# Optimization experiments

Measured on AMD Instinct MI355X. Metric: run time of the kernel, lower is better.

## Reference

```python
import jax, jax.numpy as jnp
import numpy as np

B_, N_, D_ = 8, 1024, 64
H_, DH_ = 4, 16
DI_, DS_, DTR_ = 128, 64, 4
MAXP = 512


def _ln(x, w, b, eps=1e-5):
    m = jnp.mean(x, -1, keepdims=True)
    v = jnp.mean((x - m) ** 2, -1, keepdims=True)
    return (x - m) * jax.lax.rsqrt(v + eps) * w + b


def _attn(x, drop_mask, Wq, Wkv, Wo, bo, rel_emb):
    b, n, d = x.shape
    scale = DH_ ** -0.5
    q = (x @ Wq).reshape(b, n, H_, DH_).transpose(0, 2, 1, 3)
    kv = x @ Wkv
    k = kv[..., :d].reshape(b, n, H_, DH_).transpose(0, 2, 1, 3)
    v = kv[..., d:].reshape(b, n, H_, DH_).transpose(0, 2, 1, 3)
    dots = jnp.einsum('bhid,bhjd->bhij', q, k) * scale
    seq = jnp.arange(n)
    dist = jnp.clip(seq[:, None] - seq[None, :], -MAXP, MAXP) + MAXP
    rpe = rel_emb[dist]  # (n, n, DH_)
    dots = dots + jnp.einsum('bhid,ijd->bhij', q, rpe) * scale
    # stochastic key drop: Bernoulli(0.3) positions get -1e12
    dots = dots + drop_mask.astype(dots.dtype) * (-1e12)
    attn = jax.nn.softmax(dots, axis=-1)
    out = jnp.einsum('bhij,bhjd->bhid', attn, v)
    out = out.transpose(0, 2, 1, 3).reshape(b, n, H_ * DH_)
    return out @ Wo + bo


def _mamba(x, W_in, conv_w, conv_b, W_xproj, W_dt, b_dt, A_log, Dm, W_out):
    b, n, _ = x.shape
    xz = x @ W_in                      # (b, n, 2*DI_)
    u, z = xz[..., :DI_], xz[..., DI_:]
    uc = u.transpose(0, 2, 1)          # (b, DI_, n)
    uc = jax.lax.conv_general_dilated(
        uc, conv_w[:, None, :], (1,), ((3, 0),),
        feature_group_count=DI_, dimension_numbers=('NCH', 'OIH', 'NCH'))
    uc = uc + conv_b[None, :, None]
    u = jax.nn.silu(uc).transpose(0, 2, 1)  # (b, n, DI_)
    xdb = u @ W_xproj                  # (b, n, DTR_+2*DS_)
    dt = jax.nn.softplus(xdb[..., :DTR_] @ W_dt + b_dt)  # (b, n, DI_)
    Bm = xdb[..., DTR_:DTR_ + DS_]
    Cm = xdb[..., DTR_ + DS_:]
    A = -jnp.exp(A_log)                # (DI_, DS_)

    def step(h, inp):
        dt_t, B_t, C_t, u_t = inp      # (b,DI_),(b,DS_),(b,DS_),(b,DI_)
        dA = jnp.exp(dt_t[..., None] * A)
        h = h * dA + (dt_t * u_t)[..., None] * B_t[:, None, :]
        y = jnp.einsum('bds,bs->bd', h, C_t)
        return h, y

    h0 = jnp.zeros((b, DI_, DS_), x.dtype)
    xs = (dt.transpose(1, 0, 2), Bm.transpose(1, 0, 2),
          Cm.transpose(1, 0, 2), u.transpose(1, 0, 2))
    _, ys = jax.lax.scan(step, h0, xs)
    y = ys.transpose(1, 0, 2) + u * Dm
    y = y * jax.nn.silu(z)
    return y @ W_out


def _rmsgn(x, gamma, eps=1e-5, groups=4):
    shp = x.shape
    dpg = shp[-1] // groups
    xg = x.reshape(shp[:-1] + (groups, dpg))
    rms = jnp.sqrt(jnp.sum(xg * xg, -1, keepdims=True)) * (dpg ** -0.5)
    return (xg / (rms + eps)).reshape(shp) * gamma


def _ff1(x, c1_w, c1_b, d1_w, d1_b):
    # SwiGLUConvDeconv1d(64, 256, kernel=4, shift=1); x: (b, s2, 64)
    s2 = x.shape[1]
    xc = x.transpose(0, 2, 1)
    xc = jnp.pad(xc, ((0, 0), (0, 0), (3, 3)))
    xc = jax.lax.conv_general_dilated(
        xc, c1_w, (1,), 'VALID', dimension_numbers=('NCH', 'OIH', 'NCH'))
    xc = xc + c1_b[None, :, None]
    gate = jax.nn.silu(xc[:, 256:, :])
    xc = xc[:, :256, :] * gate
    # ConvTranspose1d stride 1 == conv with flipped kernel, full padding
    w = jnp.flip(d1_w, -1).transpose(1, 0, 2)  # (64, 256, 4)
    xc = jax.lax.conv_general_dilated(
        xc, w, (1,), ((3, 3),), dimension_numbers=('NCH', 'OIH', 'NCH'))
    xc = xc + d1_b[None, :, None]
    out = xc.transpose(0, 2, 1)
    return out[:, 3:3 + s2, :]


def _forward(x, drop_mask, ln1_w, ln1_b, Wq, Wkv, Wo, bo, rel_emb,
             ln2_w, ln2_b, W_in, conv_w, conv_b, W_xproj, W_dt, b_dt,
             A_log, Dm, W_out, gamma, c1_w, c1_b, d1_w, d1_b, ln3_w, ln3_b):
    xt = _ln(x, ln1_w, ln1_b)
    xt = _attn(xt, drop_mask, Wq, Wkv, Wo, bo, rel_emb) + x
    x = x + xt  # dropout p=0 -> identity (faithful to original residual math)
    xt = _ln(x, ln2_w, ln2_b)
    m = _mamba(xt, W_in, conv_w, conv_b, W_xproj, W_dt, b_dt, A_log, Dm, W_out)
    m = jnp.where(m >= 0, m, 0.01 * m)  # leaky_relu
    m = _rmsgn(m, gamma)
    m = m + 0.5 * _ff1(m, c1_w, c1_b, d1_w, d1_b)
    x = x + m
    return _ln(x, ln3_w, ln3_b)


def setup_inputs() -> dict:
    ks = jax.random.split(jax.random.key(0), 16)
    g = lambda i, shp, s: jax.random.normal(ks[i], shp, dtype=jnp.float32) * s
    A_log = jnp.log(jnp.tile(jnp.arange(1, DS_ + 1, dtype=jnp.float32)[None, :], (DI_, 1)))
    return {
        'x': jax.random.normal(ks[0], (B_, N_, D_), dtype=jnp.float32),
        'drop_mask': jax.random.bernoulli(ks[1], 0.3, (B_, H_, N_, N_)),
        'ln1_w': jnp.ones((D_,), jnp.float32), 'ln1_b': jnp.zeros((D_,), jnp.float32),
        'Wq': g(2, (D_, D_), 0.1), 'Wkv': g(3, (D_, 2 * D_), 0.1),
        'Wo': g(4, (D_, D_), 0.1), 'bo': jnp.zeros((D_,), jnp.float32),
        'rel_emb': g(5, (2 * MAXP + 1, DH_), 0.02),
        'ln2_w': jnp.ones((D_,), jnp.float32), 'ln2_b': jnp.zeros((D_,), jnp.float32),
        'W_in': g(6, (D_, 2 * DI_), 0.1),
        'conv_w': g(7, (DI_, 4), 0.2), 'conv_b': jnp.zeros((DI_,), jnp.float32),
        'W_xproj': g(8, (DI_, DTR_ + 2 * DS_), 0.1),
        'W_dt': g(9, (DTR_, DI_), 0.1), 'b_dt': jnp.zeros((DI_,), jnp.float32),
        'A_log': A_log, 'Dm': jnp.ones((DI_,), jnp.float32),
        'W_out': g(10, (DI_, D_), 0.1),
        'gamma': jnp.ones((D_,), jnp.float32),
        'c1_w': g(11, (512, 64, 4), 0.1), 'c1_b': jnp.zeros((512,), jnp.float32),
        'd1_w': g(12, (256, 64, 4), 0.1), 'd1_b': jnp.zeros((64,), jnp.float32),
        'ln3_w': jnp.ones((D_,), jnp.float32), 'ln3_b': jnp.zeros((D_,), jnp.float32),
    }


def reference(x, drop_mask, ln1_w, ln1_b, Wq, Wkv, Wo, bo, rel_emb,
              ln2_w, ln2_b, W_in, conv_w, conv_b, W_xproj, W_dt, b_dt,
              A_log, Dm, W_out, gamma, c1_w, c1_b, d1_w, d1_b, ln3_w, ln3_b):
    return _forward(x, drop_mask, ln1_w, ln1_b, Wq, Wkv, Wo, bo, rel_emb,
                    ln2_w, ln2_b, W_in, conv_w, conv_b, W_xproj, W_dt, b_dt,
                    A_log, Dm, W_out, gamma, c1_w, c1_b, d1_w, d1_b, ln3_w, ln3_b)
```

## Files before the change

kernel.cpp:

```cpp
#include <hip/hip_runtime.h>
#include <math.h>


__device__ __forceinline__ float wsum64(float v){
#pragma unroll
  for(int m=32;m>0;m>>=1) v += __shfl_xor(v, m, 64);
  return v;
}
__device__ __forceinline__ float wmax64(float v){
#pragma unroll
  for(int m=32;m>0;m>>=1) v = fmaxf(v, __shfl_xor(v, m, 64));
  return v;
}
__device__ __forceinline__ float silu_f(float x){ return x / (1.f + __expf(-x)); }

__global__ __launch_bounds__(256) void k_ln1_qkv(
    const float* __restrict__ x, const float* __restrict__ w1, const float* __restrict__ b1,
    const float* __restrict__ Wq, const float* __restrict__ Wkv,
    const float* __restrict__ rel, const float* __restrict__ c1w,
    const int* __restrict__ dmask,
    float* __restrict__ qb, float2* __restrict__ kvT,
    float* __restrict__ relT, float* __restrict__ c1wT,
    unsigned long long* __restrict__ mask64){
  int tid = threadIdx.x;
  if (blockIdx.x >= 2048){
    size_t base = (size_t)(blockIdx.x - 2048) * 16384;
    const int* dp = dmask + base;
    unsigned long long* mp = mask64 + (base >> 6);
#pragma unroll 4
    for(int r=0;r<64;++r){
      int m = dp[r*256 + tid];
      unsigned long long bal = __ballot(m != 0);
      if ((tid & 63) == 0) mp[r*4 + (tid >> 6)] = bal;
    }
    return;
  }
  int lane = tid & 63, warp = tid >> 6;
  int token = blockIdx.x*4 + warp;
  __shared__ float xt[4][64];
  float xv = x[(size_t)token*64 + lane];
  float mean = wsum64(xv) * 0.015625f;
  float dlt = xv - mean;
  float var = wsum64(dlt*dlt) * 0.015625f;
  float xn = dlt * rsqrtf(var + 1e-5f) * w1[lane] + b1[lane];
  xt[warp][lane] = xn;
  __syncthreads();
  float aq=0.f, ak=0.f, av=0.f;
#pragma unroll 4
  for(int dd=0; dd<64; ++dd){
    float xd = xt[warp][dd];
    aq += xd * Wq[dd*64 + lane];
    ak += xd * Wkv[dd*128 + lane];
    av += xd * Wkv[dd*128 + 64 + lane];
  }
  int b = token >> 10, i = token & 1023;
  int h = lane >> 4, dh = lane & 15;
  size_t o  = (((size_t)(b*4 + h))*1024 + i)*16 + dh;
  size_t oT = (((size_t)(b*4 + h))*16 + dh)*1024 + i;
  qb[o]=aq;
  kvT[oT] = make_float2(ak, av);

  if (blockIdx.x < 65){
    int idx = blockIdx.x*256 + tid;
    if (idx < 16*1025){
      int c = idx / 1025;
      int d = idx - c*1025;
      relT[idx] = rel[d*16 + c];
    }
  } else if (blockIdx.x < 577){
    int idx = (blockIdx.x-65)*256 + tid;
    int row = idx >> 9;
    int ii  = idx & 511;
    c1wT[idx] = c1w[(size_t)ii*256 + row];
  }
}

__global__ __launch_bounds__(256) void k_kmax(
    const float2* __restrict__ kvT, float* __restrict__ Kmax){
  int tid = threadIdx.x;
  int bh = blockIdx.x;
  const float2* base = kvT + (size_t)bh*16*1024;
  float mx = 0.f;
#pragma unroll
  for(int r=0;r<4;++r){
    int j = tid + 256*r;
    float ss = 0.f;
#pragma unroll
    for(int c=0;c<16;++c){ float2 kv = base[c*1024 + j]; ss += kv.x*kv.x; }
    mx = fmaxf(mx, ss);
  }
  mx = wmax64(mx);
  __shared__ float red[4];
  int lane = tid&63, wv = tid>>6;
  if(lane==0) red[wv]=mx;
  __syncthreads();
  if(tid==0) Kmax[bh] = sqrtf(fmaxf(fmaxf(red[0],red[1]),fmaxf(red[2],red[3])));
}

__global__ __launch_bounds__(128, 2) void k_attn(
    const float* __restrict__ qb, const float2* __restrict__ kvT,
    const unsigned long long* __restrict__ mask64, const float* __restrict__ relT,
    const float* __restrict__ Kmax, float* __restrict__ attn_raw){
  int tid = threadIdx.x;
  int lane = tid & 63, wv = tid >> 6;
  int wg   = blockIdx.x;
  int xcd  = wg & 7;
  int slot = wg >> 3;
  int bh   = xcd*4 + (slot >> 7);
  int i0   = (slot & 127) * 8;
  int b = bh >> 2, h = bh & 3;
  int R0 = wv*4, R1 = R0+1, R2 = R0+2, R3 = R0+3;

  __shared__ float Gc[8][1032];
  __shared__ float qs[8][16];
  __shared__ float G0s[8], G1024s[8];
  __shared__ float gmS[8];
  __shared__ float Ms[8];
  __shared__ float sums[8];

  {
    int r = tid >> 4, c = tid & 15;
    qs[r][c] = qb[((size_t)bh*1024 + i0 + r)*16 + c] * 0.25f;
  }
  __syncthreads();

#pragma unroll 1
  for(int bb=0; bb<9; ++bb){
    int d = tid + 128*bb;
    if (d <= 1024){
      float rl[16];
#pragma unroll
      for(int c=0;c<16;++c) rl[c] = relT[c*1025 + d];
#pragma unroll
      for(int r=0;r<8;++r){
        float g = 0.f;
#pragma unroll
        for(int c=0;c<16;++c) g += qs[r][c]*rl[c];
        if (d == 0)        G0s[r] = g;
        else if (d == 1024) G1024s[r] = g;
        else {
          int j = i0 + r + 512 - d;
          if (j >= 0 && j < 1024) Gc[r][j] = g;
        }
      }
    }
  }
  __syncthreads();
  {
    const unsigned long long* mrow = mask64 + ((size_t)bh*1024 + i0)*16;
#pragma unroll 1
    for(int r=0;r<8;++r){
      float g0 = G0s[r], g1 = G1024s[r];
      int lo = i0 + r - 512;
      int hi = i0 + r + 512;
#pragma unroll
      for(int p=0;p<8;++p){
        int j = tid + 128*p;
        unsigned long long w = mrow[r*16 + (j>>6)];
        float g;
        if (j >= hi) g = g0;
        else if (j <= lo) g = g1;
        else g = Gc[r][j];
        if ((w >> (j & 63)) & 1ULL) g = -1e30f;
        Gc[r][j] = g;
      }
    }
  }
  __syncthreads();
  {
    int r = tid >> 4, l4 = tid & 15;
    float gm = -3.0e38f;
#pragma unroll
    for(int k=0;k<64;++k) gm = fmaxf(gm, Gc[r][l4 + 16*k]);
#pragma unroll
    for(int m=1;m<16;m<<=1) gm = fmaxf(gm, __shfl_xor(gm, m, 64));
    if (l4 == 0) gmS[r] = gm;
  }
  __syncthreads();
  if (tid < 8){
    float qn = 0.f;
#pragma unroll
    for(int c=0;c<16;++c) qn += qs[tid][c]*qs[tid][c];
    Ms[tid] = gmS[tid] + sqrtf(qn)*Kmax[bh];
  }
  __syncthreads();

  float q0[16], q1[16], q2[16], q3[16];
#pragma unroll
  for(int c=0;c<16;++c){ q0[c]=qs[R0][c]; q1[c]=qs[R1][c]; q2[c]=qs[R2][c]; q3[c]=qs[R3][c]; }
  float M0 = Ms[R0], M1 = Ms[R1], M2 = Ms[R2], M3 = Ms[R3];

  const float2* kvb = kvT + (size_t)bh*16*1024;

  float s0=0.f, s1=0.f, s2=0.f, s3=0.f;
  float a0[16], a1[16], a2[16], a3[16];
#pragma unroll
  for(int c=0;c<16;++c){ a0[c]=0.f; a1[c]=0.f; a2[c]=0.f; a3[c]=0.f; }

  float2 kvA[16], kvB[16];
  int j = lane;
#pragma unroll
  for(int c=0;c<16;++c) kvA[c] = kvb[c*1024 + j];

#define ATTN_STEP(KV, JJ) do {                                              \
    float sv0 = Gc[R0][JJ], sv1 = Gc[R1][JJ], sv2 = Gc[R2][JJ], sv3 = Gc[R3][JJ]; \
    _Pragma("unroll")                                                       \
    for(int c=0;c<16;++c){                                                  \
      float kx = KV[c].x;                                                   \
      sv0 += q0[c]*kx; sv1 += q1[c]*kx; sv2 += q2[c]*kx; sv3 += q3[c]*kx;   \
    }                                                                       \
    float p0 = __expf(sv0 - M0), p1 = __expf(sv1 - M1);                     \
    float p2 = __expf(sv2 - M2), p3 = __expf(sv3 - M3);                     \
    s0 += p0; s1 += p1; s2 += p2; s3 += p3;                                 \
    _Pragma("unroll")                                                       \
    for(int c=0;c<16;++c){                                                  \
      float vy = KV[c].y;                                                   \
      a0[c] += p0*vy; a1[c] += p1*vy; a2[c] += p2*vy; a3[c] += p3*vy;       \
    }                                                                       \
  } while(0)

#pragma unroll 1
  for(int t=0;t<16;t+=2){
    int jb = (j + 64) & 1023;
#pragma unroll
    for(int c=0;c<16;++c) kvB[c] = kvb[c*1024 + jb];
    ATTN_STEP(kvA, j);
    int ja = (jb + 64) & 1023;
#pragma unroll
    for(int c=0;c<16;++c) kvA[c] = kvb[c*1024 + ja];
    ATTN_STEP(kvB, jb);
    j = ja;
  }
#undef ATTN_STEP

  s0 = wsum64(s0); s1 = wsum64(s1); s2 = wsum64(s2); s3 = wsum64(s3);
#pragma unroll
  for(int c=0;c<16;++c){
    float x0 = a0[c]; x0 += __shfl_xor(x0,32,64); x0 += __shfl_xor(x0,16,64); a0[c] = x0;
    float x1 = a1[c]; x1 += __shfl_xor(x1,32,64); x1 += __shfl_xor(x1,16,64); a1[c] = x1;
    float x2 = a2[c]; x2 += __shfl_xor(x2,32,64); x2 += __shfl_xor(x2,16,64); a2[c] = x2;
    float x3 = a3[c]; x3 += __shfl_xor(x3,32,64); x3 += __shfl_xor(x3,16,64); a3[c] = x3;
  }
  __syncthreads();
  float* red = &Gc[0][0];
  if (lane < 16){
#pragma unroll
    for(int c=0;c<16;++c){
      red[R0*272 + lane*17 + c] = a0[c];
      red[R1*272 + lane*17 + c] = a1[c];
      red[R2*272 + lane*17 + c] = a2[c];
      red[R3*272 + lane*17 + c] = a3[c];
    }
  }
  if (lane == 0){ sums[R0]=s0; sums[R1]=s1; sums[R2]=s2; sums[R3]=s3; }
  __syncthreads();
  {
    int row = tid >> 4, c = tid & 15;
    float tot = 0.f;
#pragma unroll
    for(int g=0; g<16; ++g) tot += red[row*272 + g*17 + c];
    attn_raw[((size_t)b*1024 + i0 + row)*64 + h*16 + c] = tot / sums[row];
  }
}

__global__ __launch_bounds__(256) void k_post_attn(
    const float* __restrict__ x, const float* __restrict__ attn_raw,
    const float* __restrict__ Wo, const float* __restrict__ bo,
    const float* __restrict__ ln2w, const float* __restrict__ ln2b,
    const float* __restrict__ W_in,
    float* __restrict__ x2, float* __restrict__ u0, float* __restrict__ zsarr){
  int tid = threadIdx.x;
  int lane = tid & 63, wv = tid >> 6;
  int tok0 = blockIdx.x * 16;
  __shared__ float arS[16][64];
  __shared__ float lnS[16][64];
  for(int l = tid; l < 1024; l += 256)
    arS[l >> 6][l & 63] = attn_raw[(size_t)tok0*64 + l];
  __syncthreads();
#pragma unroll 1
  for(int tt = 0; tt < 4; ++tt){
    int tl = wv*4 + tt;
    int token = tok0 + tl;
    float acc = bo[lane];
#pragma unroll 4
    for(int dd = 0; dd < 64; ++dd) acc += arS[tl][dd] * Wo[dd*64 + lane];
    float t = 2.f*x[(size_t)token*64 + lane] + acc;
    x2[(size_t)token*64 + lane] = t;
    float mean = wsum64(t)*0.015625f;
    float dlt = t - mean;
    float var = wsum64(dlt*dlt)*0.015625f;
    lnS[tl][lane] = dlt*rsqrtf(var+1e-5f)*ln2w[lane] + ln2b[lane];
  }
  __syncthreads();
  int oc = tid;
  float w[64];
#pragma unroll
  for(int dd = 0; dd < 64; ++dd) w[dd] = W_in[dd*256 + oc];
  const float4* lnS4 = (const float4*)&lnS[0][0];
#pragma unroll 1
  for(int tl = 0; tl < 16; ++tl){
    float acc = 0.f;
#pragma unroll
    for(int d4 = 0; d4 < 16; ++d4){
      float4 l4 = lnS4[tl*16 + d4];
      acc += l4.x*w[4*d4] + l4.y*w[4*d4+1] + l4.z*w[4*d4+2] + l4.w*w[4*d4+3];
    }
    int token = tok0 + tl;
    if (oc < 128) u0[(size_t)token*128 + oc] = acc;
    else          zsarr[(size_t)token*128 + (oc-128)] = silu_f(acc);
  }
}

__global__ __launch_bounds__(256) void k_conv_proj(
    const float* __restrict__ u0, const float* __restrict__ conv_w, const float* __restrict__ conv_b,
    const float* __restrict__ W_xproj, const float* __restrict__ W_dt, const float* __restrict__ b_dt,
    float* __restrict__ uarr, float* __restrict__ Bmp, float* __restrict__ Cmp, float* __restrict__ dtarr){
  int sub = threadIdx.x >> 7, c = threadIdx.x & 127;
  int token = blockIdx.x*2 + sub;
  int b = token >> 10, i = token & 1023;
  __shared__ float us[2][128];
  __shared__ float dtin[2][4];
  float acc = conv_b[c];
#pragma unroll
  for(int k2=0;k2<4;++k2){
    int t2 = i - 3 + k2;
    if (t2 >= 0) acc += u0[((size_t)b*1024 + t2)*128 + c]*conv_w[c*4+k2];
  }
  float uv = silu_f(acc);
  uarr[(size_t)token*128 + c] = uv;
  us[sub][c] = uv;
  __syncthreads();
  float accA = 0.f, accB = 0.f;
  int cB = 128 + (c & 3);
#pragma unroll 4
  for(int dd=0; dd<128; ++dd){
    float xd = us[sub][dd];
    accA += xd * W_xproj[dd*132 + c];
    accB += xd * W_xproj[dd*132 + cB];
  }
  if (c < 4){ dtin[sub][c] = accA; Cmp[(size_t)token*64 + 60 + c] = accB; }
  else if (c < 68) Bmp[(size_t)token*64 + (c-4)] = accA;
  else             Cmp[(size_t)token*64 + (c-68)] = accA;
  __syncthreads();
  float dv = b_dt[c];
#pragma unroll
  for(int r2=0;r2<4;++r2) dv += dtin[sub][r2]*W_dt[r2*128 + c];
  dv = fmaxf(dv, 0.f) + log1pf(expf(-fabsf(dv)));
  dtarr[(size_t)token*128 + c] = dv;
}

__global__ __launch_bounds__(256) void k_scan_a(
    const float* __restrict__ dtarr, const float* __restrict__ uarr,
    const float* __restrict__ Bmp, const float* __restrict__ A_log,
    float* __restrict__ Parr, float* __restrict__ Rarr){
  int lane = threadIdx.x & 63, warp = threadIdx.x >> 6;
  int w = blockIdx.x*4 + warp;
  int c = w & 7, d = (w >> 3) & 127, b = w >> 10;
  float A = -expf(A_log[d*64 + lane]);
  int tb = c*128;
  const float* dtp = dtarr + ((size_t)b*1024 + tb)*128 + d;
  const float* up  = uarr  + ((size_t)b*1024 + tb)*128 + d;
  const float* Bp  = Bmp   + ((size_t)b*1024 + tb)*64 + lane;
  float R = 0.f, sdt = 0.f;
  for(int t0=0; t0<128; t0+=8){
    float dtc[8], uc[8], Bc[8];
#pragma unroll
    for(int r=0;r<8;++r){
      dtc[r]=dtp[(size_t)(t0+r)*128]; uc[r]=up[(size_t)(t0+r)*128]; Bc[r]=Bp[(size_t)(t0+r)*64];
    }
#pragma unroll
    for(int r=0;r<8;++r){
      float dt = dtc[r];
      R = R*__expf(dt*A) + dt*uc[r]*Bc[r];
      sdt += dt;
    }
  }
  Parr[(size_t)w*64 + lane] = __expf(sdt*A);
  Rarr[(size_t)w*64 + lane] = R;
}

__global__ __launch_bounds__(256) void k_scan_c(
    const float* __restrict__ dtarr, const float* __restrict__ uarr,
    const float* __restrict__ Bmp, const float* __restrict__ Cmp,
    const float* __restrict__ zsarr, const float* __restrict__ A_log,
    const float* __restrict__ Dm, const float* __restrict__ Parr,
    const float* __restrict__ Rarr, float* __restrict__ ymp){
  int lane = threadIdx.x & 63, warp = threadIdx.x >> 6;
  int w = blockIdx.x*4 + warp;
  int c = w & 7, d = (w >> 3) & 127, b = w >> 10;
  float A = -expf(A_log[d*64 + lane]);
  float Dv = Dm[d];
  float h = 0.f;
  int wbase = w - c;
#pragma unroll 1
  for(int cp=0; cp<c; ++cp){
    float P = Parr[(size_t)(wbase+cp)*64 + lane];
    float R = Rarr[(size_t)(wbase+cp)*64 + lane];
    h = h*P + R;
  }
  int tb = c*128;
  const float* dtp = dtarr + ((size_t)b*1024 + tb)*128 + d;
  const float* up  = uarr  + ((size_t)b*1024 + tb)*128 + d;
  const float* zp  = zsarr + ((size_t)b*1024 + tb)*128 + d;
  const float* Bp  = Bmp   + ((size_t)b*1024 + tb)*64 + lane;
  const float* Cp  = Cmp   + ((size_t)b*1024 + tb)*64 + lane;
  float* yp        = ymp   + ((size_t)b*1024 + tb)*128 + d;
  for(int t0=0; t0<128; t0+=8){
    float dtc[8], uc[8], Bc[8], Cc[8], zc[8];
#pragma unroll
    for(int r=0;r<8;++r){
      dtc[r]=dtp[(size_t)(t0+r)*128]; uc[r]=up[(size_t)(t0+r)*128];
      Bc[r]=Bp[(size_t)(t0+r)*64];    Cc[r]=Cp[(size_t)(t0+r)*64];
      zc[r]=zp[(size_t)(t0+r)*128];
    }
    float hc[8];
#pragma unroll
    for(int r=0;r<8;++r){
      float dt = dtc[r];
      h = h*__expf(dt*A) + dt*uc[r]*Bc[r];
      hc[r] = h*Cc[r];
    }
    float y[8];
#pragma unroll
    for(int r=0;r<8;++r) y[r] = wsum64(hc[r]);
    if (lane==0){
#pragma unroll
      for(int r=0;r<8;++r) yp[(size_t)(t0+r)*128] = (y[r] + uc[r]*Dv)*zc[r];
    }
  }
}

__global__ __launch_bounds__(256) void k_wout(
    const float* __restrict__ ymp, const float* __restrict__ W_out,
    const float* __restrict__ gamma, float* __restrict__ marr){
  int lane = threadIdx.x & 63, warp = threadIdx.x >> 6;
  int token = blockIdx.x*4 + warp;
  __shared__ float ys[4][128];
  ys[warp][lane]      = ymp[(size_t)token*128 + lane];
  ys[warp][lane+64]   = ymp[(size_t)token*128 + 64 + lane];
  __syncthreads();
  float acc = 0.f;
#pragma unroll 4
  for(int dd=0; dd<128; ++dd) acc += ys[warp][dd]*W_out[dd*64 + lane];
  acc = acc >= 0.f ? acc : 0.01f*acc;
  float ss = acc*acc;
#pragma unroll
  for(int m=1;m<16;m<<=1) ss += __shfl_xor(ss, m, 64);
  float rms = sqrtf(ss)*0.25f;
  marr[(size_t)token*64 + lane] = acc/(rms + 1e-5f)*gamma[lane];
}

__global__ __launch_bounds__(256) void k_h2(
    const float* __restrict__ marr, const float* __restrict__ c1wT,
    const float* __restrict__ c1b, float* __restrict__ h2){
  int b = blockIdx.y;
  int t0 = blockIdx.x * 16;
  int tid = threadIdx.x;
  __shared__ float ms[19][64];
  for(int l = tid; l < 19*64; l += 256){
    int row = l >> 6, cc = l & 63;
    int t = t0 - 3 + row;
    ms[row][cc] = (t >= 0 && t < 1024) ? marr[((size_t)b*1024 + t)*64 + cc] : 0.f;
  }
  __syncthreads();
  int i = tid;
  float acc1[16], acc2[16];
#pragma unroll
  for(int tl=0;tl<16;++tl){ acc1[tl]=0.f; acc2[tl]=0.f; }
  for(int cc=0; cc<64; ++cc){
    float mv[19];
#pragma unroll
    for(int r2=0;r2<19;++r2) mv[r2] = ms[r2][cc];
    const float* wr = c1wT + (size_t)cc*4*512;
    float wa0 = wr[      i], wa1 = wr[ 512+i], wa2 = wr[1024+i], wa3 = wr[1536+i];
    float wg0 = wr[  256+i], wg1 = wr[ 768+i], wg2 = wr[1280+i], wg3 = wr[1792+i];
#pragma unroll
    for(int tl=0; tl<16; ++tl){
      acc1[tl] += wa0*mv[tl+0] + wa1*mv[tl+1] + wa2*mv[tl+2] + wa3*mv[tl+3];
      acc2[tl] += wg0*mv[tl+0] + wg1*mv[tl+1] + wg2*mv[tl+2] + wg3*mv[tl+3];
    }
  }
  float bb1 = c1b[i], bb2 = c1b[i+256];
#pragma unroll
  for(int tl=0; tl<16; ++tl){
    int t = t0 + tl;
    if (t < 1027){
      float o1 = acc1[tl] + bb1;
      float o2 = acc2[tl] + bb2;
      h2[((size_t)b*1027 + t)*256 + i] = o1 * silu_f(o2);
    }
  }
}

__global__ __launch_bounds__(256) void k_ff_final(
    const float* __restrict__ h2, const float* __restrict__ d1w, const float* __restrict__ d1b,
    const float* __restrict__ x2, const float* __restrict__ marr,
    const float* __restrict__ ln3w, const float* __restrict__ ln3b,
    float* __restrict__ out){
  int b = blockIdx.y;
  int s0 = blockIdx.x * 16;
  int tid = threadIdx.x;
  int o = tid & 63, sg = tid >> 6;
  __shared__ float hs[19][256];
  for(int l = tid; l < 19*256; l += 256){
    int row = l >> 8, cc = l & 255;
    hs[row][cc] = h2[((size_t)b*1027 + s0 + row)*256 + cc];
  }
  __syncthreads();
  int sl = sg*4;
  float acc0=0.f, acc1=0.f, acc2=0.f, acc3=0.f;
  const float4* wb = (const float4*)d1w + o;
#pragma unroll 2
  for(int i2=0; i2<256; ++i2){
    float4 wv = wb[(size_t)i2*64];
    float h0=hs[sl+0][i2], h1=hs[sl+1][i2], h2v=hs[sl+2][i2], h3=hs[sl+3][i2];
    float h4=hs[sl+4][i2], h5=hs[sl+5][i2], h6=hs[sl+6][i2];
    acc0 += h0*wv.w + h1*wv.z + h2v*wv.y + h3*wv.x;
    acc1 += h1*wv.w + h2v*wv.z + h3*wv.y + h4*wv.x;
    acc2 += h2v*wv.w + h3*wv.z + h4*wv.y + h5*wv.x;
    acc3 += h3*wv.w + h4*wv.z + h5*wv.y + h6*wv.x;
  }
  float accs[4] = {acc0, acc1, acc2, acc3};
  float bo_ = d1b[o];
#pragma unroll
  for(int r=0;r<4;++r){
    int s = s0 + sl + r;
    size_t idx = ((size_t)b*1024 + s)*64 + o;
    float tot = x2[idx] + marr[idx] + 0.5f*(accs[r] + bo_);
    float mean = wsum64(tot)*0.015625f;
    float dlt = tot - mean;
    float var = wsum64(dlt*dlt)*0.015625f;
    out[idx] = dlt*rsqrtf(var+1e-5f)*ln3w[o] + ln3b[o];
  }
}

extern "C" void kernel_launch(void* const* d_in, const int* in_sizes, int n_in,
                              void* d_out, int out_size, void* d_ws, size_t ws_size,
                              hipStream_t stream){
  const float* x       = (const float*)d_in[0];
  const int*   dmask   = (const int*)  d_in[1];
  const float* ln1w    = (const float*)d_in[2];
  const float* ln1b    = (const float*)d_in[3];
  const float* Wq      = (const float*)d_in[4];
  const float* Wkv     = (const float*)d_in[5];
  const float* Wo      = (const float*)d_in[6];
  const float* bo      = (const float*)d_in[7];
  const float* rel     = (const float*)d_in[8];
  const float* ln2w    = (const float*)d_in[9];
  const float* ln2b    = (const float*)d_in[10];
  const float* W_in    = (const float*)d_in[11];
  const float* conv_w  = (const float*)d_in[12];
  const float* conv_b  = (const float*)d_in[13];
  const float* W_xproj = (const float*)d_in[14];
  const float* W_dt    = (const float*)d_in[15];
  const float* b_dt    = (const float*)d_in[16];
  const float* A_log   = (const float*)d_in[17];
  const float* Dm      = (const float*)d_in[18];
  const float* W_out   = (const float*)d_in[19];
  const float* gamma   = (const float*)d_in[20];
  const float* c1w     = (const float*)d_in[21];
  const float* c1b     = (const float*)d_in[22];
  const float* d1w     = (const float*)d_in[23];
  const float* d1b     = (const float*)d_in[24];
  const float* ln3w    = (const float*)d_in[25];
  const float* ln3b    = (const float*)d_in[26];
  float* outp = (float*)d_out;

  float* ws = (float*)d_ws;
  float* qb       = ws;
  float* kvT      = qb      + 524288;
  float* attn_raw = kvT     + 1048576;
  float* x2       = attn_raw+ 524288;
  float* u0       = x2      + 524288;
  float* zsarr    = u0      + 1048576;
  float* uarr     = zsarr   + 1048576;
  float* dtarr    = uarr    + 1048576;
  float* Bmp      = dtarr   + 1048576;
  float* Cmp      = Bmp     + 524288;
  float* ymp      = Cmp     + 524288;
  float* marr     = ymp     + 1048576;
  float* h2       = marr    + 524288;
  float* relT     = h2      + 2103296;
  float* c1wT     = relT    + 16400;
  float* Parr     = c1wT    + 131072;
  float* Rarr     = Parr    + 524288;
  float* Kmaxa    = Rarr    + 524288;

  unsigned long long* mask64 = (unsigned long long*)h2;

  k_ln1_qkv  <<<4096, 256, 0, stream>>>(x, ln1w, ln1b, Wq, Wkv, rel, c1w, dmask,
                                        qb, (float2*)kvT, relT, c1wT, mask64);
  k_kmax     <<<32, 256, 0, stream>>>((const float2*)kvT, Kmaxa);
  k_attn     <<<4096, 128, 0, stream>>>(qb, (const float2*)kvT, mask64, relT, Kmaxa, attn_raw);
  k_post_attn<<<512, 256, 0, stream>>>(x, attn_raw, Wo, bo, ln2w, ln2b, W_in, x2, u0, zsarr);
  k_conv_proj<<<4096, 256, 0, stream>>>(u0, conv_w, conv_b, W_xproj, W_dt, b_dt, uarr, Bmp, Cmp, dtarr);
  k_scan_a   <<<2048, 256, 0, stream>>>(dtarr, uarr, Bmp, A_log, Parr, Rarr);
  k_scan_c   <<<2048, 256, 0, stream>>>(dtarr, uarr, Bmp, Cmp, zsarr, A_log, Dm, Parr, Rarr, ymp);
  k_wout     <<<2048, 256, 0, stream>>>(ymp, W_out, gamma, marr);
  k_h2       <<<dim3(65,8), 256, 0, stream>>>(marr, c1wT, c1b, h2);
  k_ff_final <<<dim3(64,8), 256, 0, stream>>>(h2, d1w, d1b, x2, marr, ln3w, ln3b, outp);
}
```

Before: 748.8 us.

## Store attention bias tile in fp16 and remap blocks for XCD locality

```diff
diff --git a/kernel.cpp b/kernel.cpp
--- a/kernel.cpp
+++ b/kernel.cpp
@@ -1,4 +1,5 @@
 #include <hip/hip_runtime.h>
+#include <hip/hip_fp16.h>
 #include <math.h>
 
 
@@ -23,8 +24,9 @@
     float* __restrict__ relT, float* __restrict__ c1wT,
     unsigned long long* __restrict__ mask64){
   int tid = threadIdx.x;
-  if (blockIdx.x >= 2048){
-    size_t base = (size_t)(blockIdx.x - 2048) * 16384;
+  int bi = blockIdx.x >> 1;
+  if (blockIdx.x & 1){
+    size_t base = (size_t)bi * 16384;
     const int* dp = dmask + base;
     unsigned long long* mp = mask64 + (base >> 6);
 #pragma unroll 4
@@ -36,7 +38,7 @@
     return;
   }
   int lane = tid & 63, warp = tid >> 6;
-  int token = blockIdx.x*4 + warp;
+  int token = bi*4 + warp;
   __shared__ float xt[4][64];
   float xv = x[(size_t)token*64 + lane];
   float mean = wsum64(xv) * 0.015625f;
@@ -60,15 +62,15 @@
   qb[o]=aq;
   kvT[oT] = make_float2(ak, av);
 
-  if (blockIdx.x < 65){
-    int idx = blockIdx.x*256 + tid;
+  if (bi < 65){
+    int idx = bi*256 + tid;
     if (idx < 16*1025){
       int c = idx / 1025;
       int d = idx - c*1025;
       relT[idx] = rel[d*16 + c];
     }
-  } else if (blockIdx.x < 577){
-    int idx = (blockIdx.x-65)*256 + tid;
+  } else if (bi < 577){
+    int idx = (bi-65)*256 + tid;
     int row = idx >> 9;
     int ii  = idx & 511;
     c1wT[idx] = c1w[(size_t)ii*256 + row];
@@ -97,7 +99,7 @@
   if(tid==0) Kmax[bh] = sqrtf(fmaxf(fmaxf(red[0],red[1]),fmaxf(red[2],red[3])));
 }
 
-__global__ __launch_bounds__(128, 2) void k_attn(
+__global__ __launch_bounds__(128, 4) void k_attn(
     const float* __restrict__ qb, const float2* __restrict__ kvT,
     const unsigned long long* __restrict__ mask64, const float* __restrict__ relT,
     const float* __restrict__ Kmax, float* __restrict__ attn_raw){
@@ -111,7 +113,7 @@
   int b = bh >> 2, h = bh & 3;
   int R0 = wv*4, R1 = R0+1, R2 = R0+2, R3 = R0+3;
 
-  __shared__ float Gc[8][1032];
+  __shared__ __align__(16) __half Gc[8][1040];
   __shared__ float qs[8][16];
   __shared__ float G0s[8], G1024s[8];
   __shared__ float gmS[8];
@@ -140,7 +142,7 @@
         else if (d == 1024) G1024s[r] = g;
         else {
           int j = i0 + r + 512 - d;
-          if (j >= 0 && j < 1024) Gc[r][j] = g;
+          if (j >= 0 && j < 1024) Gc[r][j] = __float2half_rn(g);
         }
       }
     }
@@ -160,9 +162,9 @@
         float g;
         if (j >= hi) g = g0;
         else if (j <= lo) g = g1;
-        else g = Gc[r][j];
-        if ((w >> (j & 63)) & 1ULL) g = -1e30f;
-        Gc[r][j] = g;
+        else g = __half2float(Gc[r][j]);
+        if ((w >> (j & 63)) & 1ULL) g = -60000.f;
+        Gc[r][j] = __float2half_rn(g);
       }
     }
   }
@@ -171,7 +173,7 @@
     int r = tid >> 4, l4 = tid & 15;
     float gm = -3.0e38f;
 #pragma unroll
-    for(int k=0;k<64;++k) gm = fmaxf(gm, Gc[r][l4 + 16*k]);
+    for(int k=0;k<64;++k) gm = fmaxf(gm, __half2float(Gc[r][l4 + 16*k]));
 #pragma unroll
     for(int m=1;m<16;m<<=1) gm = fmaxf(gm, __shfl_xor(gm, m, 64));
     if (l4 == 0) gmS[r] = gm;
@@ -203,7 +205,8 @@
   for(int c=0;c<16;++c) kvA[c] = kvb[c*1024 + j];
 
 #define ATTN_STEP(KV, JJ) do {                                              \
-    float sv0 = Gc[R0][JJ], sv1 = Gc[R1][JJ], sv2 = Gc[R2][JJ], sv3 = Gc[R3][JJ]; \
+    float sv0 = __half2float(Gc[R0][JJ]), sv1 = __half2float(Gc[R1][JJ]);   \
+    float sv2 = __half2float(Gc[R2][JJ]), sv3 = __half2float(Gc[R3][JJ]);   \
     _Pragma("unroll")                                                       \
     for(int c=0;c<16;++c){                                                  \
       float kx = KV[c].x;                                                   \
@@ -242,7 +245,7 @@
     float x3 = a3[c]; x3 += __shfl_xor(x3,32,64); x3 += __shfl_xor(x3,16,64); a3[c] = x3;
   }
   __syncthreads();
-  float* red = &Gc[0][0];
+  float* red = (float*)&Gc[0][0];
   if (lane < 16){
 #pragma unroll
     for(int c=0;c<16;++c){
@@ -354,8 +357,12 @@
     const float* __restrict__ Bmp, const float* __restrict__ A_log,
     float* __restrict__ Parr, float* __restrict__ Rarr){
   int lane = threadIdx.x & 63, warp = threadIdx.x >> 6;
-  int w = blockIdx.x*4 + warp;
-  int c = w & 7, d = (w >> 3) & 127, b = w >> 10;
+  int wgid = blockIdx.x;
+  int b = wgid & 7;
+  int slot = wgid >> 3;
+  int d = slot & 127;
+  int c = (slot >> 7)*4 + warp;
+  size_t pw = (size_t)b*1024 + d*8 + c;
   float A = -expf(A_log[d*64 + lane]);
   int tb = c*128;
   const float* dtp = dtarr + ((size_t)b*1024 + tb)*128 + d;
@@ -375,8 +382,8 @@
       sdt += dt;
     }
   }
-  Parr[(size_t)w*64 + lane] = __expf(sdt*A);
-  Rarr[(size_t)w*64 + lane] = R;
+  Parr[pw*64 + lane] = __expf(sdt*A);
+  Rarr[pw*64 + lane] = R;
 }
 
 __global__ __launch_bounds__(256) void k_scan_c(
@@ -386,16 +393,19 @@
     const float* __restrict__ Dm, const float* __restrict__ Parr,
     const float* __restrict__ Rarr, float* __restrict__ ymp){
   int lane = threadIdx.x & 63, warp = threadIdx.x >> 6;
-  int w = blockIdx.x*4 + warp;
-  int c = w & 7, d = (w >> 3) & 127, b = w >> 10;
+  int wgid = blockIdx.x;
+  int b = wgid & 7;
+  int slot = wgid >> 3;
+  int d = slot & 127;
+  int c = (slot >> 7)*4 + warp;
+  size_t pbase = (size_t)b*1024 + d*8;
   float A = -expf(A_log[d*64 + lane]);
   float Dv = Dm[d];
   float h = 0.f;
-  int wbase = w - c;
 #pragma unroll 1
   for(int cp=0; cp<c; ++cp){
-    float P = Parr[(size_t)(wbase+cp)*64 + lane];
-    float R = Rarr[(size_t)(wbase+cp)*64 + lane];
+    float P = Parr[(pbase+cp)*64 + lane];
+    float R = Rarr[(pbase+cp)*64 + lane];
     h = h*P + R;
   }
   int tb = c*128;
```

Result: slower. 1.157 ms (+54.5%).
